# Optimization experiments

Hardware: AMD Instinct MI355X
Metric: run time of the kernel (lower is better)

The kernel has to match this reference:

```python
import jax, jax.numpy as jnp
import numpy as np

B, N, C, H = 2, 2048, 1024, 16
HD = C // H  # head dim = 64


def setup_inputs() -> dict:
    key = jax.random.key(0)
    kq, kk, kv, km = jax.random.split(key, 4)
    q = jax.random.normal(kq, (B, N, C), dtype=jnp.float32)
    k = jax.random.normal(kk, (B, N, C), dtype=jnp.float32)
    v = jax.random.normal(kv, (B, N, C), dtype=jnp.float32)
    mask = jax.random.randint(km, (B, 1, N, N), 0, 2, dtype=jnp.int32)
    return {"q": q, "k": k, "v": v, "mask": mask}


def reference(q, k, v, mask):
    b, n, c = q.shape
    # (B, N, C) -> (B, H, N, HD)
    qh = q.reshape(b, n, H, HD).transpose(0, 2, 1, 3)
    kh = k.reshape(b, n, H, HD).transpose(0, 2, 1, 3)
    vh = v.reshape(b, n, H, HD).transpose(0, 2, 1, 3)
    scale = 1.0 / jnp.sqrt(jnp.float32(HD))
    # scores: (B, H, N, N)
    scores = jnp.einsum("bhqd,bhkd->bhqk", qh, kh) * scale
    scores = jnp.where(mask == 0, jnp.float32(-1e9), scores)
    probs = jax.nn.softmax(scores, axis=-1)
    atten = jnp.einsum("bhqk,bhkd->bhqd", probs, vh)
    # (B, H, N, HD) -> (B, N, C)
    return atten.transpose(0, 2, 1, 3).reshape(b, n, c)
```

## Files before the change

### kernel.cpp

```cpp
#include <hip/hip_runtime.h>
#include <hip/hip_bf16.h>

#define B_ 2
#define N_ 2048
#define C_ 1024
#define H_ 16
#define HD_ 64

#define KT 64
#define NT (N_ / KT)
#define TILE_E 4096
#define PSTR 72
#define NW 8
#define QB 128

typedef short s16x8 __attribute__((ext_vector_type(8)));
typedef short s16x4 __attribute__((ext_vector_type(4)));
typedef float f32x4 __attribute__((ext_vector_type(4)));

__device__ __forceinline__ ushort f2bf(float x) {
    __hip_bfloat16 h = __float2bfloat16(x);
    return *reinterpret_cast<ushort*>(&h);
}

__device__ __forceinline__ s16x8 cvt8(float4 a, float4 b) {
    union { s16x8 v; __hip_bfloat162 h[4]; } u;
    u.h[0] = __float22bfloat162_rn(float2{a.x, a.y});
    u.h[1] = __float22bfloat162_rn(float2{a.z, a.w});
    u.h[2] = __float22bfloat162_rn(float2{b.x, b.y});
    u.h[3] = __float22bfloat162_rn(float2{b.z, b.w});
    return u.v;
}

__device__ __forceinline__ void gll16(const void* g, void* l) {
    __builtin_amdgcn_global_load_lds(
        (const __attribute__((address_space(1))) unsigned*)g,
        (__attribute__((address_space(3))) unsigned*)l, 16, 0, 0);
}

__global__ __launch_bounds__(256)
void pack_mask(const int* __restrict__ M, unsigned long long* __restrict__ bits) {
    const int gw   = (blockIdx.x * 256 + threadIdx.x) >> 6;
    const int lane = threadIdx.x & 63;
#pragma unroll
    for (int it = 0; it < 16; ++it) {
        const size_t wi = (size_t)gw * 16 + it;
        unsigned long long bal = __ballot(M[wi * 64 + lane] != 0);
        if (lane == 0) bits[wi] = bal;
    }
}

__global__ __launch_bounds__(256)
void conv_k(const float* __restrict__ K, ushort* __restrict__ Kw) {
    const int gt = blockIdx.x * 256 + threadIdx.x;
    const int b  = gt >> 18;
    const int h  = (gt >> 14) & 15;
    const int n  = (gt >> 3) & 2047;
    const int db = gt & 7;
    const size_t src = (size_t)(b * N_ + n) * C_ + h * 64 + db * 8;
    float4 f0 = *(const float4*)(K + src);
    float4 f1 = *(const float4*)(K + src + 4);
    const int key = n & 63, kt = n >> 6;
    ushort* dst = Kw + (size_t)((b * H_ + h) * NT + kt) * TILE_E
                     + key * 64 + ((db ^ (key & 7)) * 8);
    *(s16x8*)dst = cvt8(f0, f1);
}

__global__ __launch_bounds__(256)
void conv_v(const float* __restrict__ V, ushort* __restrict__ Vw) {
    const int gt  = blockIdx.x * 256 + threadIdx.x;
    const int b   = gt >> 16;
    const int h   = (gt >> 12) & 15;
    const int kt  = (gt >> 7) & 31;
    const int kb4 = (gt >> 3) & 15;
    const int db  = gt & 7;
    const int key0 = kb4 * 4;
    float f[4][8];
#pragma unroll
    for (int i = 0; i < 4; ++i) {
        const size_t src = (size_t)(b * N_ + kt * 64 + key0 + i) * C_ + h * 64 + db * 8;
        *(float4*)&f[i][0] = *(const float4*)(V + src);
        *(float4*)&f[i][4] = *(const float4*)(V + src + 4);
    }
    ushort* tb = Vw + (size_t)((b * H_ + h) * NT + kt) * TILE_E;
#pragma unroll
    for (int j = 0; j < 8; ++j) {
        const int d = db * 8 + j;
        union { s16x4 v; __hip_bfloat162 h2[2]; } u;
        u.h2[0] = __float22bfloat162_rn(float2{f[0][j], f[1][j]});
        u.h2[1] = __float22bfloat162_rn(float2{f[2][j], f[3][j]});
        *(s16x4*)(tb + d * 64 + (((key0 >> 3) ^ (d & 7)) * 8) + (key0 & 7)) = u.v;
    }
}

__global__ __launch_bounds__(512, 4)
void mha_fwd(const float* __restrict__ Q, const ushort* __restrict__ Kw,
             const ushort* __restrict__ Vw, const unsigned* __restrict__ bits,
             float* __restrict__ O) {
    __shared__ ushort Kl[2][TILE_E];
    __shared__ ushort Vt[2][TILE_E];
    __shared__ ushort Pl[NW][16 * PSTR];

    const int qt   = blockIdx.x;
    const int h    = blockIdx.y;
    const int b    = blockIdx.z;
    const int tid  = threadIdx.x;
    const int w    = tid >> 6;
    const int lane = tid & 63;
    const int l16  = lane & 15;
    const int quad = lane >> 4;

    const size_t head_off = (size_t)b * N_ * C_ + (size_t)h * HD_;
    const int qb = qt * QB + w * 16;

    const float qs = 0.125f * 1.44269504088896f;
    const size_t qoff = head_off + (size_t)(qb + l16) * C_ + quad * 8;
    float4 q0 = *(const float4*)(Q + qoff);
    float4 q1 = *(const float4*)(Q + qoff + 4);
    float4 q2 = *(const float4*)(Q + qoff + 32);
    float4 q3 = *(const float4*)(Q + qoff + 36);
    q0.x*=qs; q0.y*=qs; q0.z*=qs; q0.w*=qs;
    q1.x*=qs; q1.y*=qs; q1.z*=qs; q1.w*=qs;
    q2.x*=qs; q2.y*=qs; q2.z*=qs; q2.w*=qs;
    q3.x*=qs; q3.y*=qs; q3.z*=qs; q3.w*=qs;
    const s16x8 qa0 = cvt8(q0, q1);
    const s16x8 qa1 = cvt8(q2, q3);

    f32x4 acc[4];
#pragma unroll
    for (int c = 0; c < 4; ++c) acc[c] = f32x4{0.f, 0.f, 0.f, 0.f};
    float2 ls2 = {0.f, 0.f};

    const int fbase  = l16 * 64 + ((quad ^ (l16 & 7)) * 8);
    const int pwbase = l16 * PSTR + quad * 4;
    const int prbase = l16 * PSTR + quad * 8;

    const size_t tilebase = (size_t)((b * H_ + h) * NT) * TILE_E;
    const ushort* Kg = Kw + tilebase + (size_t)tid * 8;
    const ushort* Vg = Vw + tilebase + (size_t)tid * 8;

    const unsigned* mq = bits + ((size_t)b * N_ + qb + l16) * (N_ / 32);

    gll16(Kg, &Kl[0][w * 512]);
    gll16(Vg, &Vt[0][w * 512]);
    const ushort* Kg_pf = Kg + TILE_E;
    const ushort* Vg_pf = Vg + TILE_E;

    for (int kt2 = 0; kt2 < NT; kt2 += 2) {
        const uint4 mw = *(const uint4*)mq;  mq += 4;
        const bool pf1 = (kt2 + 2 < NT);
#pragma unroll
        for (int u = 0; u < 2; ++u) {
            __syncthreads();
            if (u == 0 || pf1) {
                gll16(Kg_pf, &Kl[1 - u][w * 512]);
                gll16(Vg_pf, &Vt[1 - u][w * 512]);
                Kg_pf += TILE_E;  Vg_pf += TILE_E;
            }
            const unsigned w0 = u ? mw.z : mw.x;
            const unsigned w1 = u ? mw.w : mw.y;

            f32x4 s[4];
#pragma unroll
            for (int t = 0; t < 4; ++t) {
                s16x8 kb0 = *(const s16x8*)(&Kl[u][fbase + t * 1024]);
                s16x8 kb1 = *(const s16x8*)(&Kl[u][(fbase ^ 32) + t * 1024]);
                f32x4 z = {0.f, 0.f, 0.f, 0.f};
                z = __builtin_amdgcn_mfma_f32_16x16x32_bf16(kb0, qa0, z, 0, 0, 0);
                z = __builtin_amdgcn_mfma_f32_16x16x32_bf16(kb1, qa1, z, 0, 0, 0);
                s[t] = z;
            }

            const unsigned a0 = w0 >> (quad * 4);
            const unsigned a1 = w1 >> (quad * 4);
#pragma unroll
            for (int t = 0; t < 4; ++t) {
                const unsigned aw = (t < 2) ? a0 : a1;
                const int sh = (t & 1) * 16;
                float p0 = exp2f(((aw >> (sh + 0)) & 1u) ? s[t][0] : -1e9f);
                float p1 = exp2f(((aw >> (sh + 1)) & 1u) ? s[t][1] : -1e9f);
                float p2 = exp2f(((aw >> (sh + 2)) & 1u) ? s[t][2] : -1e9f);
                float p3 = exp2f(((aw >> (sh + 3)) & 1u) ? s[t][3] : -1e9f);
                ls2.x += p0 + p2;
                ls2.y += p1 + p3;
                union { s16x4 v; __hip_bfloat162 h2[2]; } uu;
                uu.h2[0] = __float22bfloat162_rn(float2{p0, p1});
                uu.h2[1] = __float22bfloat162_rn(float2{p2, p3});
                *(s16x4*)(&Pl[w][pwbase + t * 16]) = uu.v;
            }

#pragma unroll
            for (int half = 0; half < 2; ++half) {
                s16x8 pa = *(const s16x8*)(&Pl[w][prbase + half * 32]);
#pragma unroll
                for (int c = 0; c < 4; ++c) {
                    const int vidx = (half ? (fbase ^ 32) : fbase) + c * 1024;
                    s16x8 vb = *(const s16x8*)(&Vt[u][vidx]);
                    acc[c] = __builtin_amdgcn_mfma_f32_16x16x32_bf16(pa, vb, acc[c], 0, 0, 0);
                }
            }
        }
    }

    float lsum = ls2.x + ls2.y;
    lsum += __shfl_xor(lsum, 16);
    lsum += __shfl_xor(lsum, 32);

#pragma unroll
    for (int r = 0; r < 4; ++r) {
        const float inv = 1.0f / __shfl(lsum, quad * 4 + r);
        const size_t obase = head_off + (size_t)(qb + quad * 4 + r) * C_;
        O[obase + l16]      = acc[0][r] * inv;
        O[obase + l16 + 16] = acc[1][r] * inv;
        O[obase + l16 + 32] = acc[2][r] * inv;
        O[obase + l16 + 48] = acc[3][r] * inv;
    }
}

#define KSTR 72
#define VSTR 72
__global__ __launch_bounds__(512, 4)
void mha_fwd_fb(const float* __restrict__ Q, const float* __restrict__ K,
                const float* __restrict__ V, const unsigned* __restrict__ bits,
                float* __restrict__ O) {
    __shared__ ushort Kl[2][KT * KSTR];
    __shared__ ushort Vt[2][HD_ * VSTR];
    __shared__ ushort Pl[NW][16 * PSTR];
    const int qt = blockIdx.x, h = blockIdx.y, b = blockIdx.z, tid = threadIdx.x;
    const int w = tid >> 6, lane = tid & 63, l16 = lane & 15, quad = lane >> 4;
    const size_t head_off = (size_t)b * N_ * C_ + (size_t)h * HD_;
    const int qb = qt * QB + w * 16;
    const float qs = 0.125f * 1.44269504088896f;
    const size_t qoff = head_off + (size_t)(qb + l16) * C_ + quad * 8;
    float4 q0 = *(const float4*)(Q + qoff);
    float4 q1 = *(const float4*)(Q + qoff + 4);
    float4 q2 = *(const float4*)(Q + qoff + 32);
    float4 q3 = *(const float4*)(Q + qoff + 36);
    q0.x*=qs; q0.y*=qs; q0.z*=qs; q0.w*=qs;
    q1.x*=qs; q1.y*=qs; q1.z*=qs; q1.w*=qs;
    q2.x*=qs; q2.y*=qs; q2.z*=qs; q2.w*=qs;
    q3.x*=qs; q3.y*=qs; q3.z*=qs; q3.w*=qs;
    const s16x8 qa0 = cvt8(q0, q1);
    const s16x8 qa1 = cvt8(q2, q3);
    f32x4 acc[4];
#pragma unroll
    for (int c = 0; c < 4; ++c) acc[c] = f32x4{0.f, 0.f, 0.f, 0.f};
    float lsum = 0.f;
    const int skey = tid >> 3, sd0 = (tid & 7) * 8;
    const int kp = tid >> 4, vd0 = (tid & 15) * 4;
    const int vcol = 2 * (kp & 3) + ((((kp >> 2) ^ (vd0 >> 3)) & 7) << 3);
    const unsigned* brow = bits + ((size_t)b * N_ + qb + l16) * (N_ / 32);
    const float SHIFT = 16.0f;
    {
        const size_t kbase = head_off + (size_t)skey * C_ + sd0;
        float4 kA = *(const float4*)(K + kbase);
        float4 kB = *(const float4*)(K + kbase + 4);
        *(s16x8*)(&Kl[0][skey * KSTR + sd0]) = cvt8(kA, kB);
        const size_t vbase = head_off + (size_t)(2 * kp) * C_ + vd0;
        float4 vA = *(const float4*)(V + vbase);
        float4 vB = *(const float4*)(V + vbase + C_);
        const float* ap = (const float*)&vA;
        const float* bp = (const float*)&vB;
#pragma unroll
        for (int i = 0; i < 4; ++i) {
            __hip_bfloat162 pr = __float22bfloat162_rn(float2{ap[i], bp[i]});
            *(unsigned*)(&Vt[0][(vd0 + i) * VSTR + vcol]) = *(unsigned*)&pr;
        }
    }
    for (int kt = 0; kt < NT; ++kt) {
        const int cur = kt & 1;
        float4 kA, kB, vA, vB;
        const bool has_next = (kt + 1 < NT);
        if (has_next) {
            const size_t kbase = head_off + (size_t)((kt + 1) * KT + skey) * C_ + sd0;
            kA = *(const float4*)(K + kbase);
            kB = *(const float4*)(K + kbase + 4);
            const size_t vbase = head_off + (size_t)((kt + 1) * KT + 2 * kp) * C_ + vd0;
            vA = *(const float4*)(V + vbase);
            vB = *(const float4*)(V + vbase + C_);
        }
        const unsigned w0 = brow[2 * kt];
        const unsigned w1 = brow[2 * kt + 1];
        __syncthreads();
        f32x4 s[4];
#pragma unroll
        for (int t = 0; t < 4; ++t) {
            s16x8 kb0 = *(const s16x8*)(&Kl[cur][(t * 16 + l16) * KSTR + quad * 8]);
            s16x8 kb1 = *(const s16x8*)(&Kl[cur][(t * 16 + l16) * KSTR + quad * 8 + 32]);
            f32x4 z = {0.f, 0.f, 0.f, 0.f};
            z = __builtin_amdgcn_mfma_f32_16x16x32_bf16(kb0, qa0, z, 0, 0, 0);
            z = __builtin_amdgcn_mfma_f32_16x16x32_bf16(kb1, qa1, z, 0, 0, 0);
            s[t] = z;
        }
        const unsigned a0 = w0 >> (quad * 4);
        const unsigned a1 = w1 >> (quad * 4);
#pragma unroll
        for (int t = 0; t < 4; ++t) {
            const unsigned aw = (t < 2) ? a0 : a1;
            const int sh = (t & 1) * 16;
            float p0 = exp2f((((aw >> (sh + 0)) & 1u) ? s[t][0] : -1e9f) - SHIFT);
            float p1 = exp2f((((aw >> (sh + 1)) & 1u) ? s[t][1] : -1e9f) - SHIFT);
            float p2 = exp2f((((aw >> (sh + 2)) & 1u) ? s[t][2] : -1e9f) - SHIFT);
            float p3 = exp2f((((aw >> (sh + 3)) & 1u) ? s[t][3] : -1e9f) - SHIFT);
            lsum += (p0 + p1) + (p2 + p3);
            union { s16x4 v; __hip_bfloat162 h2[2]; } uu;
            uu.h2[0] = __float22bfloat162_rn(float2{p0, p1});
            uu.h2[1] = __float22bfloat162_rn(float2{p2, p3});
            *(s16x4*)(&Pl[w][l16 * PSTR + t * 16 + quad * 4]) = uu.v;
        }
#pragma unroll
        for (int half = 0; half < 2; ++half) {
            s16x8 pa = *(const s16x8*)(&Pl[w][l16 * PSTR + half * 32 + quad * 8]);
#pragma unroll
            for (int c = 0; c < 4; ++c) {
                const int dr = c * 16 + l16;
                const int blk = (half * 4 + quad) ^ ((dr >> 3) & 7);
                s16x8 vb = *(const s16x8*)(&Vt[cur][dr * VSTR + blk * 8]);
                acc[c] = __builtin_amdgcn_mfma_f32_16x16x32_bf16(pa, vb, acc[c], 0, 0, 0);
            }
        }
        if (has_next) {
            *(s16x8*)(&Kl[1 - cur][skey * KSTR + sd0]) = cvt8(kA, kB);
            const float* ap = (const float*)&vA;
            const float* bp = (const float*)&vB;
#pragma unroll
            for (int i = 0; i < 4; ++i) {
                __hip_bfloat162 pr = __float22bfloat162_rn(float2{ap[i], bp[i]});
                *(unsigned*)(&Vt[1 - cur][(vd0 + i) * VSTR + vcol]) = *(unsigned*)&pr;
            }
        }
    }
    lsum += __shfl_xor(lsum, 16);
    lsum += __shfl_xor(lsum, 32);
#pragma unroll
    for (int r = 0; r < 4; ++r) {
        const float inv = 1.0f / __shfl(lsum, quad * 4 + r);
        const size_t obase = head_off + (size_t)(qb + quad * 4 + r) * C_;
        O[obase + l16]      = acc[0][r] * inv;
        O[obase + l16 + 16] = acc[1][r] * inv;
        O[obase + l16 + 32] = acc[2][r] * inv;
        O[obase + l16 + 48] = acc[3][r] * inv;
    }
}

extern "C" void kernel_launch(void* const* d_in, const int* in_sizes, int n_in,
                              void* d_out, int out_size, void* d_ws, size_t ws_size,
                              hipStream_t stream) {
    const float* q = (const float*)d_in[0];
    const float* k = (const float*)d_in[1];
    const float* v = (const float*)d_in[2];
    const int*   m = (const int*)d_in[3];
    float*       o = (float*)d_out;

    const size_t BITS_BYTES = (size_t)B_ * N_ * N_ / 8;
    const size_t KV_BYTES   = (size_t)B_ * H_ * N_ * HD_ * 2;
    const size_t NEED       = BITS_BYTES + 2 * KV_BYTES;

    unsigned long long* bits = (unsigned long long*)d_ws;
    hipLaunchKernelGGL(pack_mask, dim3(2048), dim3(256), 0, stream, m, bits);

    dim3 grid(N_ / QB, H_, B_);
    if (ws_size >= NEED) {
        ushort* kw = (ushort*)((char*)d_ws + BITS_BYTES);
        ushort* vw = (ushort*)((char*)d_ws + BITS_BYTES + KV_BYTES);
        hipLaunchKernelGGL(conv_k, dim3(2048), dim3(256), 0, stream, k, kw);
        hipLaunchKernelGGL(conv_v, dim3(512), dim3(256), 0, stream, v, vw);
        hipLaunchKernelGGL(mha_fwd, grid, dim3(512), 0, stream,
                           q, kw, vw, (const unsigned*)bits, o);
    } else {
        hipLaunchKernelGGL(mha_fwd_fb, grid, dim3(512), 0, stream,
                           q, k, v, (const unsigned*)bits, o);
    }
}
```

Measured before the change: 185.4 us.

## Process two 16-row query groups per wave with 4 waves per block

Each wave now handles 32 query rows (two 16-row groups) instead of 16, so every K and V fragment read from LDS feeds two MFMAs. The block shrinks from 8 to 4 waves, and each thread issues twice as many global-to-LDS loads per tile. An explicit vmcnt drain is added before each barrier so the async LDS loads finish before they are consumed. The aim is to halve LDS traffic per MFMA; the cost is more registers per wave and fewer waves available to hide latency.

Result: slower. 193.5 us (+4.4%).

```diff
diff --git a/kernel.cpp b/kernel.cpp
--- a/kernel.cpp
+++ b/kernel.cpp
@@ -11,7 +11,7 @@
 #define NT (N_ / KT)
 #define TILE_E 4096
 #define PSTR 72
-#define NW 8
+#define NW 4
 #define QB 128
 
 typedef short s16x8 __attribute__((ext_vector_type(8)));
@@ -36,6 +36,10 @@
     __builtin_amdgcn_global_load_lds(
         (const __attribute__((address_space(1))) unsigned*)g,
         (__attribute__((address_space(3))) unsigned*)l, 16, 0, 0);
+}
+
+__device__ __forceinline__ void vm_drain() {
+    __builtin_amdgcn_s_waitcnt(0x0F70);
 }
 
 __global__ __launch_bounds__(256)
@@ -93,13 +97,13 @@
     }
 }
 
-__global__ __launch_bounds__(512, 4)
+__global__ __launch_bounds__(256, 2)
 void mha_fwd(const float* __restrict__ Q, const ushort* __restrict__ Kw,
              const ushort* __restrict__ Vw, const unsigned* __restrict__ bits,
              float* __restrict__ O) {
     __shared__ ushort Kl[2][TILE_E];
     __shared__ ushort Vt[2][TILE_E];
-    __shared__ ushort Pl[NW][16 * PSTR];
+    __shared__ ushort Pl[NW][32 * PSTR];
 
     const int qt   = blockIdx.x;
     const int h    = blockIdx.y;
@@ -111,121 +115,150 @@
     const int quad = lane >> 4;
 
     const size_t head_off = (size_t)b * N_ * C_ + (size_t)h * HD_;
-    const int qb = qt * QB + w * 16;
+    const int qb = qt * QB + w * 32;
 
     const float qs = 0.125f * 1.44269504088896f;
-    const size_t qoff = head_off + (size_t)(qb + l16) * C_ + quad * 8;
-    float4 q0 = *(const float4*)(Q + qoff);
-    float4 q1 = *(const float4*)(Q + qoff + 4);
-    float4 q2 = *(const float4*)(Q + qoff + 32);
-    float4 q3 = *(const float4*)(Q + qoff + 36);
-    q0.x*=qs; q0.y*=qs; q0.z*=qs; q0.w*=qs;
-    q1.x*=qs; q1.y*=qs; q1.z*=qs; q1.w*=qs;
-    q2.x*=qs; q2.y*=qs; q2.z*=qs; q2.w*=qs;
-    q3.x*=qs; q3.y*=qs; q3.z*=qs; q3.w*=qs;
-    const s16x8 qa0 = cvt8(q0, q1);
-    const s16x8 qa1 = cvt8(q2, q3);
-
-    f32x4 acc[4];
-#pragma unroll
-    for (int c = 0; c < 4; ++c) acc[c] = f32x4{0.f, 0.f, 0.f, 0.f};
-    float2 ls2 = {0.f, 0.f};
-
-    const int fbase  = l16 * 64 + ((quad ^ (l16 & 7)) * 8);
-    const int pwbase = l16 * PSTR + quad * 4;
-    const int prbase = l16 * PSTR + quad * 8;
+    s16x8 qa[2][2];
+#pragma unroll
+    for (int g = 0; g < 2; ++g) {
+        const size_t qoff = head_off + (size_t)(qb + g * 16 + l16) * C_ + quad * 8;
+        float4 q0 = *(const float4*)(Q + qoff);
+        float4 q1 = *(const float4*)(Q + qoff + 4);
+        float4 q2 = *(const float4*)(Q + qoff + 32);
+        float4 q3 = *(const float4*)(Q + qoff + 36);
+        q0.x*=qs; q0.y*=qs; q0.z*=qs; q0.w*=qs;
+        q1.x*=qs; q1.y*=qs; q1.z*=qs; q1.w*=qs;
+        q2.x*=qs; q2.y*=qs; q2.z*=qs; q2.w*=qs;
+        q3.x*=qs; q3.y*=qs; q3.z*=qs; q3.w*=qs;
+        qa[g][0] = cvt8(q0, q1);
+        qa[g][1] = cvt8(q2, q3);
+    }
+
+    f32x4 acc[2][4];
+#pragma unroll
+    for (int g = 0; g < 2; ++g)
+#pragma unroll
+        for (int c = 0; c < 4; ++c) acc[g][c] = f32x4{0.f, 0.f, 0.f, 0.f};
+    float2 ls2[2] = {{0.f, 0.f}, {0.f, 0.f}};
+
+    const int fbase = l16 * 64 + ((quad ^ (l16 & 7)) * 8);
+    const int pwb0  = l16 * PSTR + quad * 4;
+    const int pwb1  = (16 + l16) * PSTR + quad * 4;
+    const int prb0  = l16 * PSTR + quad * 8;
+    const int prb1  = (16 + l16) * PSTR + quad * 8;
 
     const size_t tilebase = (size_t)((b * H_ + h) * NT) * TILE_E;
     const ushort* Kg = Kw + tilebase + (size_t)tid * 8;
     const ushort* Vg = Vw + tilebase + (size_t)tid * 8;
 
-    const unsigned* mq = bits + ((size_t)b * N_ + qb + l16) * (N_ / 32);
-
-    gll16(Kg, &Kl[0][w * 512]);
-    gll16(Vg, &Vt[0][w * 512]);
+    const unsigned* mq0 = bits + ((size_t)b * N_ + qb + l16) * (N_ / 32);
+    const unsigned* mq1 = mq0 + (size_t)16 * (N_ / 32);
+
+    gll16(Kg,        &Kl[0][w * 512]);
+    gll16(Kg + 2048, &Kl[0][w * 512 + 2048]);
+    gll16(Vg,        &Vt[0][w * 512]);
+    gll16(Vg + 2048, &Vt[0][w * 512 + 2048]);
     const ushort* Kg_pf = Kg + TILE_E;
     const ushort* Vg_pf = Vg + TILE_E;
 
     for (int kt2 = 0; kt2 < NT; kt2 += 2) {
-        const uint4 mw = *(const uint4*)mq;  mq += 4;
+        const uint4 mwa = *(const uint4*)mq0;  mq0 += 4;
+        const uint4 mwb = *(const uint4*)mq1;  mq1 += 4;
         const bool pf1 = (kt2 + 2 < NT);
 #pragma unroll
         for (int u = 0; u < 2; ++u) {
+            vm_drain();
             __syncthreads();
             if (u == 0 || pf1) {
-                gll16(Kg_pf, &Kl[1 - u][w * 512]);
-                gll16(Vg_pf, &Vt[1 - u][w * 512]);
+                gll16(Kg_pf,        &Kl[1 - u][w * 512]);
+                gll16(Kg_pf + 2048, &Kl[1 - u][w * 512 + 2048]);
+                gll16(Vg_pf,        &Vt[1 - u][w * 512]);
+                gll16(Vg_pf + 2048, &Vt[1 - u][w * 512 + 2048]);
                 Kg_pf += TILE_E;  Vg_pf += TILE_E;
             }
-            const unsigned w0 = u ? mw.z : mw.x;
-            const unsigned w1 = u ? mw.w : mw.y;
-
-            f32x4 s[4];
+            const unsigned w0g0 = u ? mwa.z : mwa.x;
+            const unsigned w1g0 = u ? mwa.w : mwa.y;
+            const unsigned w0g1 = u ? mwb.z : mwb.x;
+            const unsigned w1g1 = u ? mwb.w : mwb.y;
+
+            f32x4 s[2][4];
 #pragma unroll
             for (int t = 0; t < 4; ++t) {
                 s16x8 kb0 = *(const s16x8*)(&Kl[u][fbase + t * 1024]);
                 s16x8 kb1 = *(const s16x8*)(&Kl[u][(fbase ^ 32) + t * 1024]);
-                f32x4 z = {0.f, 0.f, 0.f, 0.f};
-                z = __builtin_amdgcn_mfma_f32_16x16x32_bf16(kb0, qa0, z, 0, 0, 0);
-                z = __builtin_amdgcn_mfma_f32_16x16x32_bf16(kb1, qa1, z, 0, 0, 0);
-                s[t] = z;
-            }
-
-            const unsigned a0 = w0 >> (quad * 4);
-            const unsigned a1 = w1 >> (quad * 4);
-#pragma unroll
-            for (int t = 0; t < 4; ++t) {
-                const unsigned aw = (t < 2) ? a0 : a1;
-                const int sh = (t & 1) * 16;
-                float p0 = exp2f(((aw >> (sh + 0)) & 1u) ? s[t][0] : -1e9f);
-                float p1 = exp2f(((aw >> (sh + 1)) & 1u) ? s[t][1] : -1e9f);
-                float p2 = exp2f(((aw >> (sh + 2)) & 1u) ? s[t][2] : -1e9f);
-                float p3 = exp2f(((aw >> (sh + 3)) & 1u) ? s[t][3] : -1e9f);
-                ls2.x += p0 + p2;
-                ls2.y += p1 + p3;
-                union { s16x4 v; __hip_bfloat162 h2[2]; } uu;
-                uu.h2[0] = __float22bfloat162_rn(float2{p0, p1});
-                uu.h2[1] = __float22bfloat162_rn(float2{p2, p3});
-                *(s16x4*)(&Pl[w][pwbase + t * 16]) = uu.v;
+#pragma unroll
+                for (int g = 0; g < 2; ++g) {
+                    f32x4 z = {0.f, 0.f, 0.f, 0.f};
+                    z = __builtin_amdgcn_mfma_f32_16x16x32_bf16(kb0, qa[g][0], z, 0, 0, 0);
+                    z = __builtin_amdgcn_mfma_f32_16x16x32_bf16(kb1, qa[g][1], z, 0, 0, 0);
+                    s[g][t] = z;
+                }
+            }
+
+#pragma unroll
+            for (int g = 0; g < 2; ++g) {
+                const unsigned a0 = (g ? w0g1 : w0g0) >> (quad * 4);
+                const unsigned a1 = (g ? w1g1 : w1g0) >> (quad * 4);
+                const int pw = g ? pwb1 : pwb0;
+#pragma unroll
+                for (int t = 0; t < 4; ++t) {
+                    const unsigned aw = (t < 2) ? a0 : a1;
+                    const int sh = (t & 1) * 16;
+                    float p0 = exp2f(((aw >> (sh + 0)) & 1u) ? s[g][t][0] : -1e9f);
+                    float p1 = exp2f(((aw >> (sh + 1)) & 1u) ? s[g][t][1] : -1e9f);
+                    float p2 = exp2f(((aw >> (sh + 2)) & 1u) ? s[g][t][2] : -1e9f);
+                    float p3 = exp2f(((aw >> (sh + 3)) & 1u) ? s[g][t][3] : -1e9f);
+                    ls2[g].x += p0 + p2;
+                    ls2[g].y += p1 + p3;
+                    union { s16x4 v; __hip_bfloat162 h2[2]; } uu;
+                    uu.h2[0] = __float22bfloat162_rn(float2{p0, p1});
+                    uu.h2[1] = __float22bfloat162_rn(float2{p2, p3});
+                    *(s16x4*)(&Pl[w][pw + t * 16]) = uu.v;
+                }
             }
 
 #pragma unroll
             for (int half = 0; half < 2; ++half) {
-                s16x8 pa = *(const s16x8*)(&Pl[w][prbase + half * 32]);
+                s16x8 pa0 = *(const s16x8*)(&Pl[w][prb0 + half * 32]);
+                s16x8 pa1 = *(const s16x8*)(&Pl[w][prb1 + half * 32]);
 #pragma unroll
                 for (int c = 0; c < 4; ++c) {
                     const int vidx = (half ? (fbase ^ 32) : fbase) + c * 1024;
                     s16x8 vb = *(const s16x8*)(&Vt[u][vidx]);
-                    acc[c] = __builtin_amdgcn_mfma_f32_16x16x32_bf16(pa, vb, acc[c], 0, 0, 0);
+                    acc[0][c] = __builtin_amdgcn_mfma_f32_16x16x32_bf16(pa0, vb, acc[0][c], 0, 0, 0);
+                    acc[1][c] = __builtin_amdgcn_mfma_f32_16x16x32_bf16(pa1, vb, acc[1][c], 0, 0, 0);
                 }
             }
         }
     }
 
-    float lsum = ls2.x + ls2.y;
-    lsum += __shfl_xor(lsum, 16);
-    lsum += __shfl_xor(lsum, 32);
-
-#pragma unroll
-    for (int r = 0; r < 4; ++r) {
-        const float inv = 1.0f / __shfl(lsum, quad * 4 + r);
-        const size_t obase = head_off + (size_t)(qb + quad * 4 + r) * C_;
-        O[obase + l16]      = acc[0][r] * inv;
-        O[obase + l16 + 16] = acc[1][r] * inv;
-        O[obase + l16 + 32] = acc[2][r] * inv;
-        O[obase + l16 + 48] = acc[3][r] * inv;
+#pragma unroll
+    for (int g = 0; g < 2; ++g) {
+        float lsum = ls2[g].x + ls2[g].y;
+        lsum += __shfl_xor(lsum, 16);
+        lsum += __shfl_xor(lsum, 32);
+#pragma unroll
+        for (int r = 0; r < 4; ++r) {
+            const float inv = 1.0f / __shfl(lsum, quad * 4 + r);
+            const size_t obase = head_off + (size_t)(qb + g * 16 + quad * 4 + r) * C_;
+            O[obase + l16]      = acc[g][0][r] * inv;
+            O[obase + l16 + 16] = acc[g][1][r] * inv;
+            O[obase + l16 + 32] = acc[g][2][r] * inv;
+            O[obase + l16 + 48] = acc[g][3][r] * inv;
+        }
     }
 }
 
 #define KSTR 72
 #define VSTR 72
+#define FNW 8
 __global__ __launch_bounds__(512, 4)
 void mha_fwd_fb(const float* __restrict__ Q, const float* __restrict__ K,
                 const float* __restrict__ V, const unsigned* __restrict__ bits,
                 float* __restrict__ O) {
     __shared__ ushort Kl[2][KT * KSTR];
     __shared__ ushort Vt[2][HD_ * VSTR];
-    __shared__ ushort Pl[NW][16 * PSTR];
+    __shared__ ushort Pl[FNW][16 * PSTR];
     const int qt = blockIdx.x, h = blockIdx.y, b = blockIdx.z, tid = threadIdx.x;
     const int w = tid >> 6, lane = tid & 63, l16 = lane & 15, quad = lane >> 4;
     const size_t head_off = (size_t)b * N_ * C_ + (size_t)h * HD_;
@@ -365,7 +398,7 @@
         ushort* vw = (ushort*)((char*)d_ws + BITS_BYTES + KV_BYTES);
         hipLaunchKernelGGL(conv_k, dim3(2048), dim3(256), 0, stream, k, kw);
         hipLaunchKernelGGL(conv_v, dim3(512), dim3(256), 0, stream, v, vw);
-        hipLaunchKernelGGL(mha_fwd, grid, dim3(512), 0, stream,
+        hipLaunchKernelGGL(mha_fwd, grid, dim3(256), 0, stream,
                            q, kw, vw, (const unsigned*)bits, o);
     } else {
         hipLaunchKernelGGL(mha_fwd_fb, grid, dim3(512), 0, stream,
```
